# Performance work log

Hardware: AMD Instinct MI355X
Metric: run time of the kernel (lower is better)

## Reference

```python
import jax, jax.numpy as jnp
import numpy as np

B, L, D = 4096, 50, 128          # users, neighbors/user, embed_dim
N_U, N_I, N_R, N_T = 10000, 100000, 6, 1000
EPS = 1e-5                       # BatchNorm eps (eval mode, running stats)


def setup_inputs() -> dict:
    key = jax.random.key(0)
    ks = iter(jax.random.split(key, 80))
    nk = lambda: next(ks)

    def lin(din, dout):
        s = 1.0 / np.sqrt(din)
        w = jax.random.uniform(nk(), (din, dout), minval=-s, maxval=s, dtype=jnp.float32)
        b = jax.random.uniform(nk(), (dout,), minval=-s, maxval=s, dtype=jnp.float32)
        return w, b

    inp = {}
    # embedding tables (u2e/i2e/r2e/t2e)
    inp['u2e'] = 0.1 * jax.random.normal(nk(), (N_U, D), jnp.float32)
    inp['i2e'] = 0.1 * jax.random.normal(nk(), (N_I, D), jnp.float32)
    inp['r2e'] = 0.1 * jax.random.normal(nk(), (N_R, D), jnp.float32)
    inp['t2e'] = 0.1 * jax.random.normal(nk(), (N_T, D), jnp.float32)
    # neighbor transform MLP
    inp['ne_w'], inp['ne_b'] = lin(3 * D, D)
    inp['ne1_w'], inp['ne1_b'] = lin(D, D)
    # attention MLP (NewAttention: concat(neigh, user) -> D -> D -> 1, softmax over neighbors)
    inp['att1_w'], inp['att1_b'] = lin(2 * D, D)
    inp['att2_w'], inp['att2_b'] = lin(D, D)
    inp['att3_w'], inp['att3_b'] = lin(D, 1)
    # head
    inp['lin_w'], inp['lin_b'] = lin(2 * D, D)
    inp['w1_w'], inp['w1_b'] = lin(D, D // 4)
    inp['bn1_g'] = jnp.ones((D // 4,), jnp.float32)
    inp['bn1_b'] = jnp.zeros((D // 4,), jnp.float32)
    inp['bn1_m'] = 0.1 * jax.random.normal(nk(), (D // 4,), jnp.float32)
    inp['bn1_v'] = jax.random.uniform(nk(), (D // 4,), minval=0.5, maxval=1.5, dtype=jnp.float32)
    inp['w2_w'], inp['w2_b'] = lin(D // 4, D // 8)
    inp['bn2_g'] = jnp.ones((D // 8,), jnp.float32)
    inp['bn2_b'] = jnp.zeros((D // 8,), jnp.float32)
    inp['bn2_m'] = 0.1 * jax.random.normal(nk(), (D // 8,), jnp.float32)
    inp['bn2_v'] = jax.random.uniform(nk(), (D // 8,), minval=0.5, maxval=1.5, dtype=jnp.float32)
    inp['w3_w'], inp['w3_b'] = lin(D // 8, 1)
    # index inputs (padded-fixed neighbor lists)
    inp['user_idx'] = jax.random.randint(nk(), (B,), 0, N_U)
    inp['item_idx'] = jax.random.randint(nk(), (B, L), 0, N_I)
    inp['rat_idx'] = jax.random.randint(nk(), (B, L), 0, N_R)
    inp['time_idx'] = jax.random.randint(nk(), (B, L), 0, N_T)
    return inp


def reference(u2e, i2e, r2e, t2e, ne_w, ne_b, ne1_w, ne1_b,
              att1_w, att1_b, att2_w, att2_b, att3_w, att3_b,
              lin_w, lin_b, w1_w, w1_b, bn1_g, bn1_b, bn1_m, bn1_v,
              w2_w, w2_b, bn2_g, bn2_b, bn2_m, bn2_v, w3_w, w3_b,
              user_idx, item_idx, rat_idx, time_idx):
    u = u2e[user_idx]                                                   # [B, D]
    neigh = jnp.concatenate([i2e[item_idx], r2e[rat_idx], t2e[time_idx]], axis=-1)  # [B, L, 3D]
    x = jax.nn.relu(neigh @ ne_w + ne_b)                                # [B, L, D]
    x = jax.nn.relu(x @ ne1_w + ne1_b)                                  # [B, L, D]
    # attention over neighbors, conditioned on the user embedding
    a = jnp.concatenate([x, jnp.broadcast_to(u[:, None, :], x.shape)], axis=-1)  # [B, L, 2D]
    a = jax.nn.relu(a @ att1_w + att1_b)
    a = jax.nn.relu(a @ att2_w + att2_b)
    att = jax.nn.softmax((a @ att3_w + att3_b)[..., 0], axis=-1)        # [B, L]
    pooled = jnp.einsum('bl,bld->bd', att, x)                           # torch.mm(x.t(), att).t()
    comb = jax.nn.relu(jnp.concatenate([u, pooled], axis=-1) @ lin_w + lin_b)  # [B, D]
    h = comb @ w1_w + w1_b
    h = jax.nn.relu((h - bn1_m) * jax.lax.rsqrt(bn1_v + EPS) * bn1_g + bn1_b)
    h = h @ w2_w + w2_b
    h = jax.nn.relu((h - bn2_m) * jax.lax.rsqrt(bn2_v + EPS) * bn2_g + bn2_b)
    return (h @ w3_w + w3_b)[:, 0]                                      # [B]
```

## Files before the change

### kernel.cpp

```cpp
#include <hip/hip_runtime.h>
#include <hip/hip_bf16.h>

typedef __bf16 bf16x8 __attribute__((ext_vector_type(8)));
typedef float  f32x4  __attribute__((ext_vector_type(4)));

#define W_OFF 0
#define A_OFF 16384
#define X_OFF 46080
#define SMALL 75776
#define SMEM_TOTAL 80384
#define WCHUNK 16384
#define WHALF  8192

#define WS_WPREP 0
#define WS_PI    262144
#define WS_PT    (WS_PI + 25600000)
#define WS_PR    (WS_PT + 512000)
#define WS_PU    (WS_PR + 3072)
#define WS_PU2   (WS_PU + 5120000)

__global__ void prep_weights_kernel(const float* __restrict__ ne_w,
                                    const float* __restrict__ ne1_w,
                                    const float* __restrict__ att1_w,
                                    const float* __restrict__ att2_w,
                                    const float* __restrict__ lin_w,
                                    __hip_bfloat16* __restrict__ wout) {
  __shared__ float tile[64][65];
  const int bx = blockIdx.x;
  const int c = bx >> 2, kt = (bx >> 1) & 1, ntile = bx & 1;
  const float* src; int koff;
  if      (c < 3)  { src = ne_w;   koff = c * 128; }
  else if (c == 3) { src = ne1_w;  koff = 0; }
  else if (c == 4) { src = att1_w; koff = 0; }
  else if (c == 5) { src = att2_w; koff = 0; }
  else if (c == 6) { src = att1_w; koff = 128; }
  else             { src = lin_w;  koff = 0; }
  const int tx = threadIdx.x, ty = threadIdx.y;
#pragma unroll
  for (int r = 0; r < 16; ++r) {
    int k = kt * 64 + r * 4 + ty, n = ntile * 64 + tx;
    tile[r * 4 + ty][tx] = src[(koff + k) * 128 + n];
  }
  __syncthreads();
#pragma unroll
  for (int r = 0; r < 16; ++r) {
    int n = ntile * 64 + r * 4 + ty, k = kt * 64 + tx;
    int h = k >> 6, k64 = k & 63;
    int off = c * WCHUNK + h * WHALF + n * 64 + ((((k64 >> 3) ^ (n & 7))) << 3) + (k64 & 7);
    wout[off] = __float2bfloat16(tile[tx][r * 4 + ty]);
  }
}

__device__ __forceinline__ unsigned short bf_bits(float x) {
  return __builtin_bit_cast(unsigned short, __float2bfloat16(x));
}

__device__ __forceinline__ void mfma_half2(const __hip_bfloat16* sIn,
                                           const __hip_bfloat16* sWh,
                                           f32x4 acc[2][4], int h, int m32, int nh,
                                           int lane) {
  const int mr = lane & 15;
  const int kq = lane >> 4;
#pragma unroll
  for (int ks = 0; ks < 2; ++ks) {
    const int kb16 = h * 8 + ks * 4 + kq;
    const int aswz = ((kb16 ^ mr) << 3);
    bf16x8 a0 = *(const bf16x8*)(sIn + (m32 * 32 + mr) * 128 + aswz);
    bf16x8 a1 = *(const bf16x8*)(sIn + (m32 * 32 + 16 + mr) * 128 + aswz);
    const int swzb = (((ks * 4 + kq) ^ (mr & 7)) << 3);
#pragma unroll
    for (int nt = 0; nt < 4; ++nt) {
      const int n = nh * 64 + nt * 16 + mr;
      bf16x8 b = *(const bf16x8*)(sWh + n * 64 + swzb);
      acc[0][nt] = __builtin_amdgcn_mfma_f32_16x16x32_bf16(a0, b, acc[0][nt], 0, 0, 0);
      acc[1][nt] = __builtin_amdgcn_mfma_f32_16x16x32_bf16(a1, b, acc[1][nt], 0, 0, 0);
    }
  }
}

__device__ __forceinline__ void epilogue2(f32x4 acc[2][4], const float* __restrict__ bias,
                                          const float* addvec, __hip_bfloat16* sOut,
                                          int m32, int nh, int lane) {
  const int mr = lane & 15;
  const int u = m32 >> 1;
#pragma unroll
  for (int mt = 0; mt < 2; ++mt) {
    const int rb = m32 * 32 + mt * 16 + ((lane >> 4) << 2);
#pragma unroll
    for (int nt = 0; nt < 4; ++nt) {
      const int col = nh * 64 + nt * 16 + mr;
      float bv = bias[col];
      if (addvec) bv += addvec[u * 128 + col];
      const int cblk = col >> 3, clo = col & 7;
#pragma unroll
      for (int r = 0; r < 4; ++r) {
        const int row = rb + r;
        if ((row & 63) < 50) {
          float v = fmaxf(acc[mt][nt][r] + bv, 0.0f);
          sOut[row * 128 + ((cblk ^ (row & 15)) << 3) + clo] = __float2bfloat16(v);
        }
      }
    }
  }
}

__global__ __launch_bounds__(512) void pgemm_kernel(
    const float* __restrict__ i2e, const float* __restrict__ r2e,
    const float* __restrict__ t2e, const float* __restrict__ u2e,
    const float* __restrict__ ne_b, const __hip_bfloat16* __restrict__ wprep,
    __hip_bfloat16* __restrict__ Pi, float* __restrict__ Pt, float* __restrict__ Pr,
    float* __restrict__ Pu, float* __restrict__ Pu2) {
  __shared__ __align__(16) __hip_bfloat16 sW[WCHUNK];
  __shared__ __align__(16) __hip_bfloat16 sA[64 * 128];
  const int tid = threadIdx.x, lane = tid & 63, wid = tid >> 6;
  const int m16 = wid & 3, nh = wid >> 2;
  const int bx = blockIdx.x;
  const float* src; const __hip_bfloat16* W; float* dst = nullptr;
  const float* addb = nullptr; bool bf_out = false;
  long rows0; int nrows;
  if (bx < 391)      { src = i2e; W = wprep + 0 * WCHUNK; bf_out = true; rows0 = (long)bx * 256;         nrows = 100000; }
  else if (bx < 395) { src = t2e; W = wprep + 2 * WCHUNK; dst = Pt;  rows0 = (long)(bx - 391) * 256; nrows = 1000; }
  else if (bx < 396) { src = r2e; W = wprep + 1 * WCHUNK; dst = Pr;  rows0 = 0;                      nrows = 6; addb = ne_b; }
  else if (bx < 436) { src = u2e; W = wprep + 6 * WCHUNK; dst = Pu;  rows0 = (long)(bx - 396) * 256; nrows = 10000; }
  else               { src = u2e; W = wprep + 7 * WCHUNK; dst = Pu2; rows0 = (long)(bx - 436) * 256; nrows = 10000; }

#pragma unroll
  for (int i = 0; i < 4; ++i) {
    int g = tid + i * 512;
    __builtin_amdgcn_global_load_lds(
        (__attribute__((address_space(1))) void*)(void*)(W + g * 8),
        (__attribute__((address_space(3))) void*)(void*)(sW + g * 8), 16, 0, 0);
  }
  const float4* s4 = (const float4*)src;
  const int mr = lane & 15;
  const int rb = m16 * 16 + ((lane >> 4) << 2);

  for (int t = 0; t < 4; ++t) {
    const long r0 = rows0 + t * 64;
#pragma unroll
    for (int i = 0; i < 2; ++i) {
      int g = tid + i * 512;
      int row = g >> 4, kb = g & 15;
      float4 v0 = {0.f, 0.f, 0.f, 0.f}, v1 = {0.f, 0.f, 0.f, 0.f};
      if (r0 + row < nrows) {
        long base = (r0 + row) * 32 + kb * 2;
        v0 = s4[base]; v1 = s4[base + 1];
      }
      uint4 pk;
      pk.x = ((unsigned)bf_bits(v0.y) << 16) | bf_bits(v0.x);
      pk.y = ((unsigned)bf_bits(v0.w) << 16) | bf_bits(v0.z);
      pk.z = ((unsigned)bf_bits(v1.y) << 16) | bf_bits(v1.x);
      pk.w = ((unsigned)bf_bits(v1.w) << 16) | bf_bits(v1.z);
      *(uint4*)(sA + row * 128 + ((kb ^ (row & 15)) << 3)) = pk;
    }
    __syncthreads();

    f32x4 acc[4];
#pragma unroll
    for (int j = 0; j < 4; ++j) acc[j] = (f32x4){0.f, 0.f, 0.f, 0.f};
    {
      const int kq = lane >> 4;
#pragma unroll
      for (int h = 0; h < 2; ++h) {
        const __hip_bfloat16* sWh = sW + h * WHALF;
#pragma unroll
        for (int ks = 0; ks < 2; ++ks) {
          const int kb16 = h * 8 + ks * 4 + kq;
          bf16x8 a = *(const bf16x8*)(sA + (m16 * 16 + mr) * 128 + ((kb16 ^ mr) << 3));
          const int swzb = (((ks * 4 + kq) ^ (mr & 7)) << 3);
#pragma unroll
          for (int nt = 0; nt < 4; ++nt) {
            const int n = nh * 64 + nt * 16 + mr;
            bf16x8 b = *(const bf16x8*)(sWh + n * 64 + swzb);
            acc[nt] = __builtin_amdgcn_mfma_f32_16x16x32_bf16(a, b, acc[nt], 0, 0, 0);
          }
        }
      }
    }
#pragma unroll
    for (int nt = 0; nt < 4; ++nt) {
      const int col = nh * 64 + nt * 16 + mr;
      const float bv = addb ? addb[col] : 0.f;
#pragma unroll
      for (int r = 0; r < 4; ++r) {
        const int row = rb + r;
        if (r0 + row < nrows) {
          if (bf_out) Pi[(r0 + row) * 128 + col] = __float2bfloat16(acc[nt][r]);
          else        dst[(r0 + row) * 128 + col] = acc[nt][r] + bv;
        }
      }
    }
    __syncthreads();
  }
}

__global__ __launch_bounds__(512, 4) void graphdec_main(
    const __hip_bfloat16* __restrict__ Pi, const float* __restrict__ Pt,
    const float* __restrict__ Pr, const float* __restrict__ Pu,
    const float* __restrict__ Pu2,
    const float* __restrict__ ne1_b, const float* __restrict__ att1_b,
    const float* __restrict__ att2_b, const float* __restrict__ att3_w,
    const float* __restrict__ lin_w, const float* __restrict__ lin_b,
    const float* __restrict__ w1_w, const float* __restrict__ w1_b,
    const float* __restrict__ bn1_g, const float* __restrict__ bn1_b,
    const float* __restrict__ bn1_m, const float* __restrict__ bn1_v,
    const float* __restrict__ w2_w, const float* __restrict__ w2_b,
    const float* __restrict__ bn2_g, const float* __restrict__ bn2_b,
    const float* __restrict__ bn2_m, const float* __restrict__ bn2_v,
    const float* __restrict__ w3_w, const float* __restrict__ w3_b,
    const int* __restrict__ user_idx, const int* __restrict__ item_idx,
    const int* __restrict__ rat_idx, const int* __restrict__ time_idx,
    const __hip_bfloat16* __restrict__ wprep, float* __restrict__ out) {
  __shared__ __align__(16) unsigned char smem[SMEM_TOTAL];
  __hip_bfloat16* sW = (__hip_bfloat16*)(smem + W_OFF);
  __hip_bfloat16* sA = (__hip_bfloat16*)(smem + A_OFF);
  __hip_bfloat16* sX = (__hip_bfloat16*)(smem + X_OFF);
  int*   sIdx   = (int*)  (smem + SMALL);
  float* sUatt  = (float*)(smem + SMALL + 1536);
  float* sUlin  = (float*)(smem + SMALL + 2560);
  float* sLP0   = (float*)(smem + SMALL + 3584);
  float* sLP1   = (float*)(smem + SMALL + 4096);
  float* sPool4 = (float*)(smem + W_OFF);
  float* sCombP = (float*)(smem + W_OFF + 2048);
  float* sAtt   = (float*)(smem + W_OFF + 4096);
  float* sPooled= (float*)(smem + W_OFF + 4608);
  float* sComb  = (float*)(smem + W_OFF + 5632);
  float* sH1    = (float*)(smem + W_OFF + 6656);

  const int tid  = threadIdx.x;
  const int lane = tid & 63;
  const int wid  = tid >> 6;
  const int m32  = wid & 3;
  const int nh   = wid >> 2;
  const int b    = blockIdx.x;

  float att3r[4];
#pragma unroll
  for (int nt = 0; nt < 4; ++nt) att3r[nt] = att3_w[nh * 64 + nt * 16 + (lane & 15)];

  if (tid < 384) {
    int c = tid >> 7, rest = tid & 127, u = rest >> 6, l = rest & 63;
    int v = 0;
    if (l < 50) {
      const int* p = (c == 0) ? item_idx : (c == 1) ? rat_idx : time_idx;
      v = p[(2 * b + u) * 50 + l];
    }
    sIdx[tid] = v;
  }
  {
    int u = tid >> 8, r = tid & 255;
    const long uidu = user_idx[2 * b + u];
    if (r < 128) sUatt[u * 128 + r]         = Pu [uidu * 128 + r];
    else         sUlin[u * 128 + (r - 128)] = Pu2[uidu * 128 + (r - 128)];
  }
  __syncthreads();

  auto stage16 = [&](const __hip_bfloat16* __restrict__ src) {
#pragma unroll
    for (int i = 0; i < 2; ++i) {
      int g = tid + i * 512;
      __builtin_amdgcn_global_load_lds(
          (__attribute__((address_space(1))) void*)(void*)(src + g * 8),
          (__attribute__((address_space(3))) void*)(void*)(sW + g * 8), 16, 0, 0);
    }
  };

  f32x4 acc[2][4];
  const f32x4 zf = {0.f, 0.f, 0.f, 0.f};
  auto zacc = [&]() {
#pragma unroll
    for (int i = 0; i < 2; ++i)
#pragma unroll
      for (int j = 0; j < 4; ++j) acc[i][j] = zf;
  };

  stage16(wprep + 3 * WCHUNK);
#pragma unroll
  for (int i = 0; i < 4; ++i) {
    int g = tid + i * 512;
    if (g < 1664) {
      int u = (g >= 832) ? 1 : 0;
      int gl = g - u * 832;
      int l = gl >> 4, kb = gl & 15;
      uint4 pk = {0u, 0u, 0u, 0u};
      if (l < 50) {
        const bf16x8 pv = *(const bf16x8*)(Pi + (long)sIdx[u * 64 + l] * 128 + kb * 8);
        const float4* pr4 = (const float4*)(Pr + (long)sIdx[128 + u * 64 + l] * 128) + kb * 2;
        const float4* pt4 = (const float4*)(Pt + (long)sIdx[256 + u * 64 + l] * 128) + kb * 2;
        float4 r0 = pr4[0], r1 = pr4[1];
        float4 t0 = pt4[0], t1 = pt4[1];
        float s0 = fmaxf((float)pv[0] + r0.x + t0.x, 0.f);
        float s1 = fmaxf((float)pv[1] + r0.y + t0.y, 0.f);
        float s2 = fmaxf((float)pv[2] + r0.z + t0.z, 0.f);
        float s3 = fmaxf((float)pv[3] + r0.w + t0.w, 0.f);
        float s4 = fmaxf((float)pv[4] + r1.x + t1.x, 0.f);
        float s5 = fmaxf((float)pv[5] + r1.y + t1.y, 0.f);
        float s6 = fmaxf((float)pv[6] + r1.z + t1.z, 0.f);
        float s7 = fmaxf((float)pv[7] + r1.w + t1.w, 0.f);
        pk.x = ((unsigned)bf_bits(s1) << 16) | bf_bits(s0);
        pk.y = ((unsigned)bf_bits(s3) << 16) | bf_bits(s2);
        pk.z = ((unsigned)bf_bits(s5) << 16) | bf_bits(s4);
        pk.w = ((unsigned)bf_bits(s7) << 16) | bf_bits(s6);
      }
      const int row = u * 64 + l;
      *(uint4*)(sA + row * 128 + ((kb ^ (row & 15)) << 3)) = pk;
    }
  }
  __syncthreads();

  zacc();
  mfma_half2(sA, sW, acc, 0, m32, nh, lane);
  __syncthreads();
  stage16(wprep + 3 * WCHUNK + WHALF);
  __syncthreads();
  mfma_half2(sA, sW, acc, 1, m32, nh, lane);
  __syncthreads();
  stage16(wprep + 4 * WCHUNK);
  epilogue2(acc, ne1_b, nullptr, sX, m32, nh, lane);
  __syncthreads();

  zacc();
  mfma_half2(sX, sW, acc, 0, m32, nh, lane);
  __syncthreads();
  stage16(wprep + 4 * WCHUNK + WHALF);
  __syncthreads();
  mfma_half2(sX, sW, acc, 1, m32, nh, lane);
  __syncthreads();
  stage16(wprep + 5 * WCHUNK);
  epilogue2(acc, att1_b, sUatt, sA, m32, nh, lane);
  __syncthreads();

  zacc();
  mfma_half2(sA, sW, acc, 0, m32, nh, lane);
  __syncthreads();
  stage16(wprep + 5 * WCHUNK + WHALF);
  __syncthreads();
  mfma_half2(sA, sW, acc, 1, m32, nh, lane);
  {
    float lp[2][4] = {{0.f, 0.f, 0.f, 0.f}, {0.f, 0.f, 0.f, 0.f}};
#pragma unroll
    for (int nt = 0; nt < 4; ++nt) {
      const int col = nh * 64 + nt * 16 + (lane & 15);
      const float b2 = att2_b[col];
#pragma unroll
      for (int mt = 0; mt < 2; ++mt)
#pragma unroll
        for (int r = 0; r < 4; ++r)
          lp[mt][r] += fmaxf(acc[mt][nt][r] + b2, 0.f) * att3r[nt];
    }
#pragma unroll
    for (int off = 1; off < 16; off <<= 1) {
#pragma unroll
      for (int mt = 0; mt < 2; ++mt)
#pragma unroll
        for (int r = 0; r < 4; ++r) lp[mt][r] += __shfl_xor(lp[mt][r], off);
    }
    if ((lane & 15) == 0) {
      float* dst = nh ? sLP1 : sLP0;
#pragma unroll
      for (int mt = 0; mt < 2; ++mt) {
        const int rowb = m32 * 32 + mt * 16 + ((lane >> 4) << 2);
#pragma unroll
        for (int r = 0; r < 4; ++r) dst[rowb + r] = lp[mt][r];
      }
    }
  }
  __syncthreads();

  if (wid < 2) {
    const int u = wid;
    float v = (lane < 50) ? (sLP0[u * 64 + lane] + sLP1[u * 64 + lane]) : -3.4e38f;
    float m = v;
    for (int off = 32; off > 0; off >>= 1) m = fmaxf(m, __shfl_xor(m, off));
    float e = (lane < 50) ? __expf(v - m) : 0.f;
    float s = e;
    for (int off = 32; off > 0; off >>= 1) s += __shfl_xor(s, off);
    sAtt[u * 64 + lane] = e / s;
  }
  __syncthreads();

  {
    int u = tid >> 8, q = (tid >> 7) & 1, d = tid & 127;
    const int cblk = d >> 3, clo = d & 7;
    float s = 0.f;
    for (int l = q; l < 50; l += 2) {
      const int row = u * 64 + l;
      s += sAtt[row] * (float)sX[row * 128 + ((cblk ^ (row & 15)) << 3) + clo];
    }
    sPool4[(u * 2 + q) * 128 + d] = s;
  }
  __syncthreads();
  if (tid < 256) {
    int u = tid >> 7, d = tid & 127;
    sPooled[u * 128 + d] = sPool4[(u * 2) * 128 + d] + sPool4[(u * 2 + 1) * 128 + d];
  }
  __syncthreads();

  {
    int u = tid >> 8, q = (tid >> 7) & 1, d = tid & 127;
    float s = 0.f;
    for (int j = q * 64; j < q * 64 + 64; ++j)
      s += sPooled[u * 128 + j] * lin_w[(128 + j) * 128 + d];
    sCombP[(u * 2 + q) * 128 + d] = s;
  }
  __syncthreads();
  if (tid < 256) {
    int u = tid >> 7, d = tid & 127;
    sComb[u * 128 + d] = fmaxf(sCombP[(u * 2) * 128 + d] + sCombP[(u * 2 + 1) * 128 + d]
                               + sUlin[u * 128 + d] + lin_b[d], 0.f);
  }
  __syncthreads();

  if (wid < 2) {
    const int u = wid;
    if (lane < 32) {
      float s = w1_b[lane];
      for (int k = 0; k < 128; ++k) s += sComb[u * 128 + k] * w1_w[k * 32 + lane];
      s = (s - bn1_m[lane]) * rsqrtf(bn1_v[lane] + 1e-5f) * bn1_g[lane] + bn1_b[lane];
      sH1[u * 32 + lane] = fmaxf(s, 0.f);
    }
    if (lane < 16) {
      float s = w2_b[lane];
      for (int k = 0; k < 32; ++k) s += sH1[u * 32 + k] * w2_w[k * 16 + lane];
      s = (s - bn2_m[lane]) * rsqrtf(bn2_v[lane] + 1e-5f) * bn2_g[lane] + bn2_b[lane];
      float p = fmaxf(s, 0.f) * w3_w[lane];
      p += __shfl_xor(p, 1); p += __shfl_xor(p, 2);
      p += __shfl_xor(p, 4); p += __shfl_xor(p, 8);
      if (lane == 0) out[2 * b + u] = p + w3_b[0];
    }
  }
}

extern "C" void kernel_launch(void* const* d_in, const int* in_sizes, int n_in,
                              void* d_out, int out_size, void* d_ws, size_t ws_size,
                              hipStream_t stream) {
  const float* u2e    = (const float*)d_in[0];
  const float* i2e    = (const float*)d_in[1];
  const float* r2e    = (const float*)d_in[2];
  const float* t2e    = (const float*)d_in[3];
  const float* ne_w   = (const float*)d_in[4];
  const float* ne_b   = (const float*)d_in[5];
  const float* ne1_w  = (const float*)d_in[6];
  const float* ne1_b  = (const float*)d_in[7];
  const float* att1_w = (const float*)d_in[8];
  const float* att1_b = (const float*)d_in[9];
  const float* att2_w = (const float*)d_in[10];
  const float* att2_b = (const float*)d_in[11];
  const float* att3_w = (const float*)d_in[12];
  const float* att3_b = (const float*)d_in[13];
  const float* lin_w  = (const float*)d_in[14];
  const float* lin_b  = (const float*)d_in[15];
  const float* w1_w   = (const float*)d_in[16];
  const float* w1_b   = (const float*)d_in[17];
  const float* bn1_g  = (const float*)d_in[18];
  const float* bn1_b  = (const float*)d_in[19];
  const float* bn1_m  = (const float*)d_in[20];
  const float* bn1_v  = (const float*)d_in[21];
  const float* w2_w   = (const float*)d_in[22];
  const float* w2_b   = (const float*)d_in[23];
  const float* bn2_g  = (const float*)d_in[24];
  const float* bn2_b  = (const float*)d_in[25];
  const float* bn2_m  = (const float*)d_in[26];
  const float* bn2_v  = (const float*)d_in[27];
  const float* w3_w   = (const float*)d_in[28];
  const float* w3_b   = (const float*)d_in[29];
  const int* user_idx = (const int*)d_in[30];
  const int* item_idx = (const int*)d_in[31];
  const int* rat_idx  = (const int*)d_in[32];
  const int* time_idx = (const int*)d_in[33];
  (void)att3_b;

  char* ws = (char*)d_ws;
  __hip_bfloat16* wprep = (__hip_bfloat16*)(ws + WS_WPREP);
  __hip_bfloat16* Pi = (__hip_bfloat16*)(ws + WS_PI);
  float* Pt  = (float*)(ws + WS_PT);
  float* Pr  = (float*)(ws + WS_PR);
  float* Pu  = (float*)(ws + WS_PU);
  float* Pu2 = (float*)(ws + WS_PU2);
  float* out = (float*)d_out;

  prep_weights_kernel<<<32, dim3(64, 4), 0, stream>>>(ne_w, ne1_w, att1_w, att2_w,
                                                      lin_w, wprep);
  pgemm_kernel<<<476, 512, 0, stream>>>(i2e, r2e, t2e, u2e, ne_b, wprep,
                                        Pi, Pt, Pr, Pu, Pu2);
  graphdec_main<<<2048, 512, 0, stream>>>(
      Pi, Pt, Pr, Pu, Pu2, ne1_b, att1_b, att2_b, att3_w,
      lin_w, lin_b, w1_w, w1_b, bn1_g, bn1_b, bn1_m, bn1_v, w2_w, w2_b,
      bn2_g, bn2_b, bn2_m, bn2_v, w3_w, w3_b,
      user_idx, item_idx, rat_idx, time_idx, wprep, out);
}
```

Baseline: 246.9 us.

## Hold MLP weight fragments in registers instead of staging through LDS

Each wave now loads its B-operand weight fragments for a whole 128x128 layer straight from global memory into 16 bf16x8 registers, and prefetches the next layer's fragments while the current epilogue runs. This removes the LDS weight buffer, the half-chunk staging, and several block-wide barriers per layer, and shrinks shared memory so more blocks can fit per CU. The cost is 64 extra VGPRs per thread under launch_bounds(512,4), which risks spilling. The w1 head matvec is also split across all threads with a partial-sum reduction instead of running on 32 lanes.

```diff
diff --git a/kernel.cpp b/kernel.cpp
--- a/kernel.cpp
+++ b/kernel.cpp
@@ -4,13 +4,13 @@
 typedef __bf16 bf16x8 __attribute__((ext_vector_type(8)));
 typedef float  f32x4  __attribute__((ext_vector_type(4)));
 
-#define W_OFF 0
-#define A_OFF 16384
-#define X_OFF 46080
-#define SMALL 75776
-#define SMEM_TOTAL 80384
 #define WCHUNK 16384
 #define WHALF  8192
+
+#define MA_OFF 0
+#define MX_OFF 29696
+#define MSMALL 59392
+#define MTOT   64000
 
 #define WS_WPREP 0
 #define WS_PI    262144
@@ -55,25 +55,43 @@
   return __builtin_bit_cast(unsigned short, __float2bfloat16(x));
 }
 
-__device__ __forceinline__ void mfma_half2(const __hip_bfloat16* sIn,
-                                           const __hip_bfloat16* sWh,
-                                           f32x4 acc[2][4], int h, int m32, int nh,
-                                           int lane) {
+__device__ __forceinline__ void load_bfrags(const __hip_bfloat16* __restrict__ gW,
+                                            bf16x8 bf[16], int nh, int lane) {
   const int mr = lane & 15;
   const int kq = lane >> 4;
 #pragma unroll
-  for (int ks = 0; ks < 2; ++ks) {
-    const int kb16 = h * 8 + ks * 4 + kq;
-    const int aswz = ((kb16 ^ mr) << 3);
-    bf16x8 a0 = *(const bf16x8*)(sIn + (m32 * 32 + mr) * 128 + aswz);
-    bf16x8 a1 = *(const bf16x8*)(sIn + (m32 * 32 + 16 + mr) * 128 + aswz);
-    const int swzb = (((ks * 4 + kq) ^ (mr & 7)) << 3);
-#pragma unroll
-    for (int nt = 0; nt < 4; ++nt) {
-      const int n = nh * 64 + nt * 16 + mr;
-      bf16x8 b = *(const bf16x8*)(sWh + n * 64 + swzb);
-      acc[0][nt] = __builtin_amdgcn_mfma_f32_16x16x32_bf16(a0, b, acc[0][nt], 0, 0, 0);
-      acc[1][nt] = __builtin_amdgcn_mfma_f32_16x16x32_bf16(a1, b, acc[1][nt], 0, 0, 0);
+  for (int h = 0; h < 2; ++h) {
+#pragma unroll
+    for (int ks = 0; ks < 2; ++ks) {
+      const int swzb = (((ks * 4 + kq) ^ (mr & 7)) << 3);
+#pragma unroll
+      for (int nt = 0; nt < 4; ++nt) {
+        const int n = nh * 64 + nt * 16 + mr;
+        bf[h * 8 + ks * 4 + nt] = *(const bf16x8*)(gW + h * WHALF + n * 64 + swzb);
+      }
+    }
+  }
+}
+
+__device__ __forceinline__ void mfma_layer(const __hip_bfloat16* sIn, const bf16x8 bf[16],
+                                           f32x4 acc[2][4], int m32, int lane) {
+  const int mr = lane & 15;
+  const int kq = lane >> 4;
+#pragma unroll
+  for (int h = 0; h < 2; ++h) {
+#pragma unroll
+    for (int ks = 0; ks < 2; ++ks) {
+      const int kb16 = h * 8 + ks * 4 + kq;
+      const int aswz = ((kb16 ^ mr) << 3);
+      bf16x8 a0 = *(const bf16x8*)(sIn + (m32 * 32 + mr) * 128 + aswz);
+      bf16x8 a1 = *(const bf16x8*)(sIn + (m32 * 32 + 16 + mr) * 128 + aswz);
+#pragma unroll
+      for (int nt = 0; nt < 4; ++nt) {
+        acc[0][nt] = __builtin_amdgcn_mfma_f32_16x16x32_bf16(a0, bf[h * 8 + ks * 4 + nt],
+                                                             acc[0][nt], 0, 0, 0);
+        acc[1][nt] = __builtin_amdgcn_mfma_f32_16x16x32_bf16(a1, bf[h * 8 + ks * 4 + nt],
+                                                             acc[1][nt], 0, 0, 0);
+      }
     }
   }
 }
@@ -211,21 +229,21 @@
     const int* __restrict__ user_idx, const int* __restrict__ item_idx,
     const int* __restrict__ rat_idx, const int* __restrict__ time_idx,
     const __hip_bfloat16* __restrict__ wprep, float* __restrict__ out) {
-  __shared__ __align__(16) unsigned char smem[SMEM_TOTAL];
-  __hip_bfloat16* sW = (__hip_bfloat16*)(smem + W_OFF);
-  __hip_bfloat16* sA = (__hip_bfloat16*)(smem + A_OFF);
-  __hip_bfloat16* sX = (__hip_bfloat16*)(smem + X_OFF);
-  int*   sIdx   = (int*)  (smem + SMALL);
-  float* sUatt  = (float*)(smem + SMALL + 1536);
-  float* sUlin  = (float*)(smem + SMALL + 2560);
-  float* sLP0   = (float*)(smem + SMALL + 3584);
-  float* sLP1   = (float*)(smem + SMALL + 4096);
-  float* sPool4 = (float*)(smem + W_OFF);
-  float* sCombP = (float*)(smem + W_OFF + 2048);
-  float* sAtt   = (float*)(smem + W_OFF + 4096);
-  float* sPooled= (float*)(smem + W_OFF + 4608);
-  float* sComb  = (float*)(smem + W_OFF + 5632);
-  float* sH1    = (float*)(smem + W_OFF + 6656);
+  __shared__ __align__(16) unsigned char smem[MTOT];
+  __hip_bfloat16* sA = (__hip_bfloat16*)(smem + MA_OFF);
+  __hip_bfloat16* sX = (__hip_bfloat16*)(smem + MX_OFF);
+  int*   sIdx  = (int*)  (smem + MSMALL);
+  float* sUatt = (float*)(smem + MSMALL + 1536);
+  float* sUlin = (float*)(smem + MSMALL + 2560);
+  float* sLP0  = (float*)(smem + MSMALL + 3584);
+  float* sLP1  = (float*)(smem + MSMALL + 4096);
+  float* sAtt   = (float*)(smem + MA_OFF);
+  float* sPool4 = (float*)(smem + MA_OFF + 512);
+  float* sPooled= (float*)(smem + MA_OFF + 2560);
+  float* sCombP = (float*)(smem + MA_OFF + 3584);
+  float* sComb  = (float*)(smem + MA_OFF + 5632);
+  float* sH1p   = (float*)(smem + MA_OFF + 6656);
+  float* sH1    = (float*)(smem + MA_OFF + 8704);
 
   const int tid  = threadIdx.x;
   const int lane = tid & 63;
@@ -238,6 +256,9 @@
 #pragma unroll
   for (int nt = 0; nt < 4; ++nt) att3r[nt] = att3_w[nh * 64 + nt * 16 + (lane & 15)];
 
+  bf16x8 bf[16];
+  load_bfrags(wprep + 3 * WCHUNK, bf, nh, lane);
+
   if (tid < 384) {
     int c = tid >> 7, rest = tid & 127, u = rest >> 6, l = rest & 63;
     int v = 0;
@@ -255,26 +276,6 @@
   }
   __syncthreads();
 
-  auto stage16 = [&](const __hip_bfloat16* __restrict__ src) {
-#pragma unroll
-    for (int i = 0; i < 2; ++i) {
-      int g = tid + i * 512;
-      __builtin_amdgcn_global_load_lds(
-          (__attribute__((address_space(1))) void*)(void*)(src + g * 8),
-          (__attribute__((address_space(3))) void*)(void*)(sW + g * 8), 16, 0, 0);
-    }
-  };
-
-  f32x4 acc[2][4];
-  const f32x4 zf = {0.f, 0.f, 0.f, 0.f};
-  auto zacc = [&]() {
-#pragma unroll
-    for (int i = 0; i < 2; ++i)
-#pragma unroll
-      for (int j = 0; j < 4; ++j) acc[i][j] = zf;
-  };
-
-  stage16(wprep + 3 * WCHUNK);
 #pragma unroll
   for (int i = 0; i < 4; ++i) {
     int g = tid + i * 512;
@@ -308,34 +309,29 @@
   }
   __syncthreads();
 
+  f32x4 acc[2][4];
+  const f32x4 zf = {0.f, 0.f, 0.f, 0.f};
+  auto zacc = [&]() {
+#pragma unroll
+    for (int i = 0; i < 2; ++i)
+#pragma unroll
+      for (int j = 0; j < 4; ++j) acc[i][j] = zf;
+  };
+
   zacc();
-  mfma_half2(sA, sW, acc, 0, m32, nh, lane);
-  __syncthreads();
-  stage16(wprep + 3 * WCHUNK + WHALF);
-  __syncthreads();
-  mfma_half2(sA, sW, acc, 1, m32, nh, lane);
-  __syncthreads();
-  stage16(wprep + 4 * WCHUNK);
+  mfma_layer(sA, bf, acc, m32, lane);
+  load_bfrags(wprep + 4 * WCHUNK, bf, nh, lane);
   epilogue2(acc, ne1_b, nullptr, sX, m32, nh, lane);
   __syncthreads();
 
   zacc();
-  mfma_half2(sX, sW, acc, 0, m32, nh, lane);
-  __syncthreads();
-  stage16(wprep + 4 * WCHUNK + WHALF);
-  __syncthreads();
-  mfma_half2(sX, sW, acc, 1, m32, nh, lane);
-  __syncthreads();
-  stage16(wprep + 5 * WCHUNK);
+  mfma_layer(sX, bf, acc, m32, lane);
+  load_bfrags(wprep + 5 * WCHUNK, bf, nh, lane);
   epilogue2(acc, att1_b, sUatt, sA, m32, nh, lane);
   __syncthreads();
 
   zacc();
-  mfma_half2(sA, sW, acc, 0, m32, nh, lane);
-  __syncthreads();
-  stage16(wprep + 5 * WCHUNK + WHALF);
-  __syncthreads();
-  mfma_half2(sA, sW, acc, 1, m32, nh, lane);
+  mfma_layer(sA, bf, acc, m32, lane);
   {
     float lp[2][4] = {{0.f, 0.f, 0.f, 0.f}, {0.f, 0.f, 0.f, 0.f}};
 #pragma unroll
@@ -411,14 +407,24 @@
   }
   __syncthreads();
 
+  {
+    int u = tid >> 8, j = (tid >> 3) & 31, q = tid & 7;
+    float s = 0.f;
+    for (int k = q * 16; k < q * 16 + 16; ++k) s += sComb[u * 128 + k] * w1_w[k * 32 + j];
+    sH1p[(u * 8 + q) * 32 + j] = s;
+  }
+  __syncthreads();
+  if (tid < 64) {
+    int u = tid >> 5, j = tid & 31;
+    float s = w1_b[j];
+#pragma unroll
+    for (int q = 0; q < 8; ++q) s += sH1p[(u * 8 + q) * 32 + j];
+    s = (s - bn1_m[j]) * rsqrtf(bn1_v[j] + 1e-5f) * bn1_g[j] + bn1_b[j];
+    sH1[u * 32 + j] = fmaxf(s, 0.f);
+  }
+  __syncthreads();
   if (wid < 2) {
     const int u = wid;
-    if (lane < 32) {
-      float s = w1_b[lane];
-      for (int k = 0; k < 128; ++k) s += sComb[u * 128 + k] * w1_w[k * 32 + lane];
-      s = (s - bn1_m[lane]) * rsqrtf(bn1_v[lane] + 1e-5f) * bn1_g[lane] + bn1_b[lane];
-      sH1[u * 32 + lane] = fmaxf(s, 0.f);
-    }
     if (lane < 16) {
       float s = w2_b[lane];
       for (int k = 0; k < 32; ++k) s += sH1[u * 32 + k] * w2_w[k * 16 + lane];
```

Result: slower. 320.2 us (+29.7%).
